# Performance work log

Hardware: AMD Instinct MI355X
Metric: run time of the kernel (lower is better)

The kernel has to match this reference:

```python
import jax, jax.numpy as jnp
import numpy as np

ENT_TOTAL = 1_000_000
REL_TOTAL = 10_000
HIDDEN = 128      # == ent_size == rel_size
REL_TYPE = 1_000
MARGIN = 1.0
BATCH = 8192


def setup_inputs() -> dict:
    key = jax.random.key(0)
    ks = jax.random.split(key, 10)
    return {
        "ent_emb": jax.random.normal(ks[0], (ENT_TOTAL, HIDDEN), jnp.float32) * 0.05,
        "rel_emb": jax.random.normal(ks[1], (REL_TOTAL, HIDDEN), jnp.float32) * 0.05,
        "type_mat": jax.random.normal(ks[2], (REL_TYPE, HIDDEN * HIDDEN), jnp.float32) * 0.05,
        "pos_h": jax.random.randint(ks[3], (BATCH,), 0, ENT_TOTAL, jnp.int64 if jax.config.jax_enable_x64 else jnp.int32),
        "pos_t": jax.random.randint(ks[4], (BATCH,), 0, ENT_TOTAL, jnp.int32),
        "pos_r": jax.random.randint(ks[5], (BATCH,), 0, REL_TOTAL, jnp.int32),
        "pos_type_r": jax.random.randint(ks[6], (BATCH,), 0, REL_TYPE, jnp.int32),
        "neg_h": jax.random.randint(ks[7], (BATCH,), 0, ENT_TOTAL, jnp.int32),
        "neg_t": jax.random.randint(ks[8], (BATCH,), 0, ENT_TOTAL, jnp.int32),
        "neg_r": jax.random.randint(ks[9], (BATCH,), 0, REL_TOTAL, jnp.int32),
    }


def _l2norm(x):
    return x * jax.lax.rsqrt(jnp.sum(x * x, axis=-1, keepdims=True) + 1e-12)


def _calc(h, t, r):
    # l2-normalize each, then |h + r - t|
    return jnp.abs(_l2norm(h) + _l2norm(r) - _l2norm(t))


def reference(ent_emb, rel_emb, type_mat, pos_h, pos_t, pos_r, pos_type_r,
              neg_h, neg_t, neg_r):
    B = pos_h.shape[0]
    D = ent_emb.shape[1]
    # gathers
    p_h = ent_emb[pos_h]                       # [B, D]
    p_t = ent_emb[pos_t]
    p_r = rel_emb[pos_r]
    n_h = ent_emb[neg_h]
    n_t = ent_emb[neg_t]
    n_r = rel_emb[neg_r]
    # per-sample transfer matrix; original code uses pos_type_r for BOTH
    # positive and negative (faithful to source).
    T = type_mat[pos_type_r].reshape(B, D, D)  # [B, ent_size, rel_size]
    # per-sample transfer: [B, D] x [B, D, R] -> [B, R]
    p_h_ = jnp.einsum('bd,bdr->br', p_h, T)
    p_t_ = jnp.einsum('bd,bdr->br', p_t, T)
    n_h_ = jnp.einsum('bd,bdr->br', n_h, T)
    n_t_ = jnp.einsum('bd,bdr->br', n_t, T)
    p_score = jnp.sum(_calc(p_h_, p_t_, p_r), axis=-1, keepdims=True)  # [B,1]
    n_score = jnp.sum(_calc(n_h_, n_t_, n_r), axis=-1, keepdims=True)
    loss = jnp.mean(jnp.maximum(p_score - n_score + MARGIN, 0.0))
    return loss
```

## Files before the change

### kernel.cpp

```cpp
#include <hip/hip_runtime.h>

#define D 128
#define MAX_B 8192
#define MARGIN 1.0f


#define BFLY5(x) { x += __shfl_xor(x, 1); x += __shfl_xor(x, 2); x += __shfl_xor(x, 4); \
                   x += __shfl_xor(x, 8); x += __shfl_xor(x, 16); }

#define FMA4(A, T, S) { (A).x = fmaf((T).x, (S), (A).x); (A).y = fmaf((T).y, (S), (A).y); \
                        (A).z = fmaf((T).z, (S), (A).z); (A).w = fmaf((T).w, (S), (A).w); }

struct SampleRegs {
    float2 e0, e1, e2, e3;
    float4 rp, rn;
};

__device__ __forceinline__ void fetch_sample(
    SampleRegs& S, int o,
    const float* __restrict__ ent, const float* __restrict__ rel,
    const int* __restrict__ pos_h, const int* __restrict__ pos_t,
    const int* __restrict__ pos_r, const int* __restrict__ neg_h,
    const int* __restrict__ neg_t, const int* __restrict__ neg_r,
    int l, int cg)
{
    const size_t b0 = (size_t)pos_h[o] * D;
    const size_t b1 = (size_t)pos_t[o] * D;
    const size_t b2 = (size_t)neg_h[o] * D;
    const size_t b3 = (size_t)neg_t[o] * D;
    const size_t r0 = (size_t)pos_r[o] * D;
    const size_t r1 = (size_t)neg_r[o] * D;
    S.e0 = *(const float2*)&ent[b0 + 2 * l];
    S.e1 = *(const float2*)&ent[b1 + 2 * l];
    S.e2 = *(const float2*)&ent[b2 + 2 * l];
    S.e3 = *(const float2*)&ent[b3 + 2 * l];
    S.rp = *(const float4*)&rel[r0 + 4 * cg];
    S.rn = *(const float4*)&rel[r1 + 4 * cg];
}

__device__ __forceinline__ void commit_sample(float* vbw, const SampleRegs& S, int l) {
    *(float2*)&vbw[0 * D + 2 * l] = S.e0;
    *(float2*)&vbw[1 * D + 2 * l] = S.e1;
    *(float2*)&vbw[2 * D + 2 * l] = S.e2;
    *(float2*)&vbw[3 * D + 2 * l] = S.e3;
}

__device__ __forceinline__ float sample_score(
    const float* __restrict__ T_lds, const float* __restrict__ vbw,
    int h, int cg, float4 rp, float4 rn)
{
    const float4* __restrict__ T4 = (const float4*)T_lds;
    const float4* __restrict__ vv = (const float4*)vbw;
    float4 a0 = make_float4(0.f, 0.f, 0.f, 0.f), a1 = a0, a2 = a0, a3 = a0;
    const int rb  = h * 64;
    const int vb0 = h * 16;
    #pragma unroll 4
    for (int dg = 0; dg < 16; ++dg) {
        const int row = rb + dg * 4;
        const float4 t0 = T4[(row + 0) * 32 + cg];
        const float4 t1 = T4[(row + 1) * 32 + cg];
        const float4 t2 = T4[(row + 2) * 32 + cg];
        const float4 t3 = T4[(row + 3) * 32 + cg];
        const int vi = vb0 + dg;
        const float4 v0 = vv[0 * 32 + vi];
        FMA4(a0, t0, v0.x); FMA4(a0, t1, v0.y); FMA4(a0, t2, v0.z); FMA4(a0, t3, v0.w);
        const float4 v1 = vv[1 * 32 + vi];
        FMA4(a1, t0, v1.x); FMA4(a1, t1, v1.y); FMA4(a1, t2, v1.z); FMA4(a1, t3, v1.w);
        const float4 v2 = vv[2 * 32 + vi];
        FMA4(a2, t0, v2.x); FMA4(a2, t1, v2.y); FMA4(a2, t2, v2.z); FMA4(a2, t3, v2.w);
        const float4 v3 = vv[3 * 32 + vi];
        FMA4(a3, t0, v3.x); FMA4(a3, t1, v3.y); FMA4(a3, t2, v3.z); FMA4(a3, t3, v3.w);
    }
    a0.x += __shfl_xor(a0.x, 32); a0.y += __shfl_xor(a0.y, 32);
    a0.z += __shfl_xor(a0.z, 32); a0.w += __shfl_xor(a0.w, 32);
    a1.x += __shfl_xor(a1.x, 32); a1.y += __shfl_xor(a1.y, 32);
    a1.z += __shfl_xor(a1.z, 32); a1.w += __shfl_xor(a1.w, 32);
    a2.x += __shfl_xor(a2.x, 32); a2.y += __shfl_xor(a2.y, 32);
    a2.z += __shfl_xor(a2.z, 32); a2.w += __shfl_xor(a2.w, 32);
    a3.x += __shfl_xor(a3.x, 32); a3.y += __shfl_xor(a3.y, 32);
    a3.z += __shfl_xor(a3.z, 32); a3.w += __shfl_xor(a3.w, 32);

    float sph = a0.x*a0.x + a0.y*a0.y + a0.z*a0.z + a0.w*a0.w;
    float spt = a1.x*a1.x + a1.y*a1.y + a1.z*a1.z + a1.w*a1.w;
    float snh = a2.x*a2.x + a2.y*a2.y + a2.z*a2.z + a2.w*a2.w;
    float snt = a3.x*a3.x + a3.y*a3.y + a3.z*a3.z + a3.w*a3.w;
    float spr = rp.x*rp.x + rp.y*rp.y + rp.z*rp.z + rp.w*rp.w;
    float snr = rn.x*rn.x + rn.y*rn.y + rn.z*rn.z + rn.w*rn.w;
    BFLY5(sph); BFLY5(spt); BFLY5(snh); BFLY5(snt); BFLY5(spr); BFLY5(snr);
    const float iph = rsqrtf(sph + 1e-12f);
    const float ipt = rsqrtf(spt + 1e-12f);
    const float inh = rsqrtf(snh + 1e-12f);
    const float itn = rsqrtf(snt + 1e-12f);
    const float ipr = rsqrtf(spr + 1e-12f);
    const float inr = rsqrtf(snr + 1e-12f);
    float z = fabsf(a0.x*iph + rp.x*ipr - a1.x*ipt)
            + fabsf(a0.y*iph + rp.y*ipr - a1.y*ipt)
            + fabsf(a0.z*iph + rp.z*ipr - a1.z*ipt)
            + fabsf(a0.w*iph + rp.w*ipr - a1.w*ipt)
            - fabsf(a2.x*inh + rn.x*inr - a3.x*itn)
            - fabsf(a2.y*inh + rn.y*inr - a3.y*itn)
            - fabsf(a2.z*inh + rn.z*inr - a3.z*itn)
            - fabsf(a2.w*inh + rn.w*inr - a3.w*itn);
    BFLY5(z);
    return fmaxf(z + MARGIN, 0.f);
}

__global__ __launch_bounds__(512, 4) void fused_kernel(
    const float* __restrict__ ent,
    const float* __restrict__ rel,
    const float* __restrict__ tmat,
    const int* __restrict__ pos_h,
    const int* __restrict__ pos_t,
    const int* __restrict__ pos_r,
    const int* __restrict__ type_r,
    const int* __restrict__ neg_h,
    const int* __restrict__ neg_t,
    const int* __restrict__ neg_r,
    float* __restrict__ out,
    int B, float inv_B)
{
    const int t   = blockIdx.x;
    const int tid = threadIdx.x;
    const int l   = tid & 63;
    const int w   = tid >> 6;
    const int cg  = l & 31;
    const int h   = l >> 5;

    __shared__ float T_lds[D * D];
    __shared__ float vbuf[8][4][D];
    int* lsc = (int*)&vbuf[0][0][0];

    float4 ts[8];
    {
        const float4* Tg = (const float4*)(tmat + (size_t)t * (D * D));
        #pragma unroll
        for (int k = 0; k < 8; ++k)
            ts[k] = Tg[tid + k * 512];
    }

    const int per = (B + 511) >> 9;
    int vals[16];
    const int base = tid * per;
    int mc = 0;
    if (per == 16 && base + 15 < B) {
        const int4* vp = (const int4*)(type_r + base);
        #pragma unroll
        for (int k = 0; k < 4; ++k) {
            const int4 v = vp[k];
            vals[4*k+0] = v.x; vals[4*k+1] = v.y;
            vals[4*k+2] = v.z; vals[4*k+3] = v.w;
        }
    } else {
        for (int j = 0; j < 16; ++j) {
            const int s = base + j;
            vals[j] = (j < per && s < B) ? type_r[s] : -1;
        }
    }
    #pragma unroll
    for (int j = 0; j < 16; ++j) mc += (vals[j] == t);

    {
        float4* Ts = (float4*)T_lds;
        #pragma unroll
        for (int k = 0; k < 8; ++k)
            Ts[tid + k * 512] = ts[k];
    }

    int inc = mc;
    #pragma unroll
    for (int off = 1; off < 64; off <<= 1) {
        const int tv = __shfl_up(inc, off);
        if (l >= off) inc += tv;
    }
    if (l == 63) lsc[64 + w] = inc;
    __syncthreads();
    int wbase = 0, cnt = 0;
    #pragma unroll
    for (int k = 0; k < 8; ++k) {
        const int s = lsc[64 + k];
        wbase += (k < w) ? s : 0;
        cnt += s;
    }
    const int excl = wbase + inc - mc;
    __syncthreads();

    float wl = 0.f;
    for (int r0 = 0;; r0 += 64) {
        {
            int g = excl;
            #pragma unroll
            for (int j = 0; j < 16; ++j) {
                if (vals[j] == t) {
                    const int wr = g - r0;
                    if (wr >= 0 && wr < 64) lsc[wr] = base + j;
                    ++g;
                }
            }
        }
        __syncthreads();
        const int wcnt = min(cnt - r0, 64);
        int sidx[8];
        int nk = 0;
        #pragma unroll
        for (int k = 0; k < 8; ++k) {
            const int rank = w + 8 * k;
            if (rank < wcnt) sidx[nk++] = lsc[rank];
        }
        __syncthreads();

        if (nk > 0) {
            float* vbw = &vbuf[w][0][0];
            SampleRegs A, Bq;
            fetch_sample(A, sidx[0], ent, rel, pos_h, pos_t, pos_r,
                         neg_h, neg_t, neg_r, l, cg);
            for (int k = 0;; ++k) {
                commit_sample(vbw, A, l);
                const bool more = (k + 1) < nk;
                if (more)
                    fetch_sample(Bq, sidx[k + 1], ent, rel, pos_h, pos_t, pos_r,
                                 neg_h, neg_t, neg_r, l, cg);
                wl += sample_score(T_lds, vbw, h, cg, A.rp, A.rn);
                if (!more) break;
                A = Bq;
            }
        }
        if (r0 + 64 >= cnt) break;
        __syncthreads();
    }

    __syncthreads();
    if (l == 0) ((float*)lsc)[w] = wl;
    __syncthreads();
    if (tid == 0) {
        float s = 0.f;
        #pragma unroll
        for (int k = 0; k < 8; ++k) s += ((float*)lsc)[k];
        if (s != 0.f) atomicAdd(out, s * inv_B);
    }
}


__global__ __launch_bounds__(128) void transr_fallback(
    const float* __restrict__ ent, const float* __restrict__ rel,
    const float* __restrict__ tmat,
    const int* __restrict__ pos_h, const int* __restrict__ pos_t,
    const int* __restrict__ pos_r, const int* __restrict__ pos_type_r,
    const int* __restrict__ neg_h, const int* __restrict__ neg_t,
    const int* __restrict__ neg_r, float* __restrict__ out, int B)
{
    const int b = blockIdx.x;
    const int r = threadIdx.x;
    const int lane = r & 63;
    const int wid = r >> 6;
    __shared__ float4 vcomb[D];
    __shared__ float sred[16];
    vcomb[r] = make_float4(ent[(size_t)pos_h[b]*D + r], ent[(size_t)pos_t[b]*D + r],
                           ent[(size_t)neg_h[b]*D + r], ent[(size_t)neg_t[b]*D + r]);
    const float prr = rel[(size_t)pos_r[b] * D + r];
    const float nrr = rel[(size_t)neg_r[b] * D + r];
    __syncthreads();
    const float* __restrict__ T = tmat + (size_t)pos_type_r[b] * (D * D);
    float aph = 0.f, apt = 0.f, anh = 0.f, ant = 0.f;
    #pragma unroll 8
    for (int d = 0; d < D; ++d) {
        const float t = T[d * D + r];
        const float4 v = vcomb[d];
        aph = fmaf(v.x, t, aph); apt = fmaf(v.y, t, apt);
        anh = fmaf(v.z, t, anh); ant = fmaf(v.w, t, ant);
    }
    float s0 = aph*aph, s1 = apt*apt, s2 = anh*anh, s3 = ant*ant;
    float s4 = prr*prr, s5 = nrr*nrr;
    #pragma unroll
    for (int off = 32; off; off >>= 1) {
        s0 += __shfl_xor(s0, off); s1 += __shfl_xor(s1, off);
        s2 += __shfl_xor(s2, off); s3 += __shfl_xor(s3, off);
        s4 += __shfl_xor(s4, off); s5 += __shfl_xor(s5, off);
    }
    if (lane == 0) {
        sred[wid*8+0]=s0; sred[wid*8+1]=s1; sred[wid*8+2]=s2;
        sred[wid*8+3]=s3; sred[wid*8+4]=s4; sred[wid*8+5]=s5;
    }
    __syncthreads();
    const float iph = rsqrtf(sred[0]+sred[8] +1e-12f);
    const float ipt = rsqrtf(sred[1]+sred[9] +1e-12f);
    const float inh = rsqrtf(sred[2]+sred[10]+1e-12f);
    const float itn = rsqrtf(sred[3]+sred[11]+1e-12f);
    const float ipr = rsqrtf(sred[4]+sred[12]+1e-12f);
    const float inr = rsqrtf(sred[5]+sred[13]+1e-12f);
    float pterm = fabsf(aph*iph + prr*ipr - apt*ipt);
    float nterm = fabsf(anh*inh + nrr*inr - ant*itn);
    #pragma unroll
    for (int off = 32; off; off >>= 1) {
        pterm += __shfl_xor(pterm, off);
        nterm += __shfl_xor(nterm, off);
    }
    __syncthreads();
    if (lane == 0) { sred[wid*2+0] = pterm; sred[wid*2+1] = nterm; }
    __syncthreads();
    if (r == 0)
        atomicAdd(out, fmaxf(sred[0]+sred[2] - sred[1]-sred[3] + MARGIN, 0.f) / (float)B);
}


extern "C" void kernel_launch(void* const* d_in, const int* in_sizes, int n_in,
                              void* d_out, int out_size, void* d_ws, size_t ws_size,
                              hipStream_t stream) {
    const float* ent  = (const float*)d_in[0];
    const float* rel  = (const float*)d_in[1];
    const float* tmat = (const float*)d_in[2];
    const int* pos_h      = (const int*)d_in[3];
    const int* pos_t      = (const int*)d_in[4];
    const int* pos_r      = (const int*)d_in[5];
    const int* pos_type_r = (const int*)d_in[6];
    const int* neg_h      = (const int*)d_in[7];
    const int* neg_t      = (const int*)d_in[8];
    const int* neg_r      = (const int*)d_in[9];
    float* out = (float*)d_out;
    const int B = in_sizes[3];
    const int ntype = in_sizes[2] / (D * D);

    hipMemsetAsync(out, 0, sizeof(float), stream);

    if (B > MAX_B) {
        transr_fallback<<<B, 128, 0, stream>>>(
            ent, rel, tmat, pos_h, pos_t, pos_r, pos_type_r,
            neg_h, neg_t, neg_r, out, B);
        return;
    }

    fused_kernel<<<ntype, 512, 0, stream>>>(
        ent, rel, tmat, pos_h, pos_t, pos_r, pos_type_r,
        neg_h, neg_t, neg_r, out, B, 1.0f / (float)B);
}
```

Baseline: 46.61 us.

## Process two relation types per block to halve grid size

Each block now handles two consecutive relation types. It counts matches for both in a single pass over type_r, packing the two counts into one int so a single prefix scan serves both. The second type's transfer matrix is loaded into LDS after the first type's samples are scored. This halves the repeated per-block scan of the 8192-entry type array and the block launch count. The cost is less parallelism (500 blocks instead of 1000) and serialized matrix loads within each block.

```diff
diff --git a/kernel.cpp b/kernel.cpp
--- a/kernel.cpp
+++ b/kernel.cpp
@@ -117,9 +117,10 @@
     const int* __restrict__ neg_t,
     const int* __restrict__ neg_r,
     float* __restrict__ out,
-    int B, float inv_B)
+    int B, int ntype, float inv_B)
 {
-    const int t   = blockIdx.x;
+    const int t0  = 2 * blockIdx.x;
+    const int t1  = t0 + 1;
     const int tid = threadIdx.x;
     const int l   = tid & 63;
     const int w   = tid >> 6;
@@ -132,7 +133,7 @@
 
     float4 ts[8];
     {
-        const float4* Tg = (const float4*)(tmat + (size_t)t * (D * D));
+        const float4* Tg = (const float4*)(tmat + (size_t)t0 * (D * D));
         #pragma unroll
         for (int k = 0; k < 8; ++k)
             ts[k] = Tg[tid + k * 512];
@@ -141,7 +142,7 @@
     const int per = (B + 511) >> 9;
     int vals[16];
     const int base = tid * per;
-    int mc = 0;
+    int mc0 = 0, mc1 = 0;
     if (per == 16 && base + 15 < B) {
         const int4* vp = (const int4*)(type_r + base);
         #pragma unroll
@@ -157,7 +158,10 @@
         }
     }
     #pragma unroll
-    for (int j = 0; j < 16; ++j) mc += (vals[j] == t);
+    for (int j = 0; j < 16; ++j) {
+        mc0 += (vals[j] == t0);
+        mc1 += (vals[j] == t1);
+    }
 
     {
         float4* Ts = (float4*)T_lds;
@@ -166,7 +170,8 @@
             Ts[tid + k * 512] = ts[k];
     }
 
-    int inc = mc;
+    const int p = mc0 | (mc1 << 16);
+    int inc = p;
     #pragma unroll
     for (int off = 1; off < 64; off <<= 1) {
         const int tv = __shfl_up(inc, off);
@@ -174,58 +179,79 @@
     }
     if (l == 63) lsc[64 + w] = inc;
     __syncthreads();
-    int wbase = 0, cnt = 0;
+    int wbase = 0, tot = 0;
     #pragma unroll
     for (int k = 0; k < 8; ++k) {
         const int s = lsc[64 + k];
         wbase += (k < w) ? s : 0;
-        cnt += s;
-    }
-    const int excl = wbase + inc - mc;
+        tot += s;
+    }
+    const int epk  = wbase + inc - p;
+    const int excl0 = epk & 0xFFFF, excl1 = (int)((unsigned)epk >> 16);
+    const int cnt0  = tot & 0xFFFF, cnt1  = (int)((unsigned)tot >> 16);
     __syncthreads();
 
     float wl = 0.f;
-    for (int r0 = 0;; r0 += 64) {
-        {
-            int g = excl;
+
+    for (int ph = 0; ph < 2; ++ph) {
+        const int t    = ph ? t1 : t0;
+        const int excl = ph ? excl1 : excl0;
+        const int cnt  = ph ? cnt1 : cnt0;
+        if (ph == 1) {
+            if (t >= ntype || cnt == 0) break;
+            const float4* Tg = (const float4*)(tmat + (size_t)t * (D * D));
+            float4 t2[8];
             #pragma unroll
-            for (int j = 0; j < 16; ++j) {
-                if (vals[j] == t) {
-                    const int wr = g - r0;
-                    if (wr >= 0 && wr < 64) lsc[wr] = base + j;
-                    ++g;
+            for (int k = 0; k < 8; ++k) t2[k] = Tg[tid + k * 512];
+            __syncthreads();
+            float4* Ts = (float4*)T_lds;
+            #pragma unroll
+            for (int k = 0; k < 8; ++k) Ts[tid + k * 512] = t2[k];
+        }
+        if (cnt == 0) continue;
+
+        for (int r0 = 0;; r0 += 64) {
+            {
+                int g = excl;
+                #pragma unroll
+                for (int j = 0; j < 16; ++j) {
+                    if (vals[j] == t) {
+                        const int wr = g - r0;
+                        if (wr >= 0 && wr < 64) lsc[wr] = base + j;
+                        ++g;
+                    }
                 }
             }
+            __syncthreads();
+            const int wcnt = min(cnt - r0, 64);
+            int sidx[8];
+            int nk = 0;
+            #pragma unroll
+            for (int k = 0; k < 8; ++k) {
+                const int rank = w + 8 * k;
+                if (rank < wcnt) sidx[nk++] = lsc[rank];
+            }
+            __syncthreads();
+
+            if (nk > 0) {
+                float* vbw = &vbuf[w][0][0];
+                SampleRegs A, Bq;
+                fetch_sample(A, sidx[0], ent, rel, pos_h, pos_t, pos_r,
+                             neg_h, neg_t, neg_r, l, cg);
+                for (int k = 0;; ++k) {
+                    commit_sample(vbw, A, l);
+                    const bool more = (k + 1) < nk;
+                    if (more)
+                        fetch_sample(Bq, sidx[k + 1], ent, rel, pos_h, pos_t,
+                                     pos_r, neg_h, neg_t, neg_r, l, cg);
+                    wl += sample_score(T_lds, vbw, h, cg, A.rp, A.rn);
+                    if (!more) break;
+                    A = Bq;
+                }
+            }
+            if (r0 + 64 >= cnt) break;
+            __syncthreads();
         }
-        __syncthreads();
-        const int wcnt = min(cnt - r0, 64);
-        int sidx[8];
-        int nk = 0;
-        #pragma unroll
-        for (int k = 0; k < 8; ++k) {
-            const int rank = w + 8 * k;
-            if (rank < wcnt) sidx[nk++] = lsc[rank];
-        }
-        __syncthreads();
-
-        if (nk > 0) {
-            float* vbw = &vbuf[w][0][0];
-            SampleRegs A, Bq;
-            fetch_sample(A, sidx[0], ent, rel, pos_h, pos_t, pos_r,
-                         neg_h, neg_t, neg_r, l, cg);
-            for (int k = 0;; ++k) {
-                commit_sample(vbw, A, l);
-                const bool more = (k + 1) < nk;
-                if (more)
-                    fetch_sample(Bq, sidx[k + 1], ent, rel, pos_h, pos_t, pos_r,
-                                 neg_h, neg_t, neg_r, l, cg);
-                wl += sample_score(T_lds, vbw, h, cg, A.rp, A.rn);
-                if (!more) break;
-                A = Bq;
-            }
-        }
-        if (r0 + 64 >= cnt) break;
-        __syncthreads();
     }
 
     __syncthreads();
@@ -263,10 +289,10 @@
     float aph = 0.f, apt = 0.f, anh = 0.f, ant = 0.f;
     #pragma unroll 8
     for (int d = 0; d < D; ++d) {
-        const float t = T[d * D + r];
+        const float tt = T[d * D + r];
         const float4 v = vcomb[d];
-        aph = fmaf(v.x, t, aph); apt = fmaf(v.y, t, apt);
-        anh = fmaf(v.z, t, anh); ant = fmaf(v.w, t, ant);
+        aph = fmaf(v.x, tt, aph); apt = fmaf(v.y, tt, apt);
+        anh = fmaf(v.z, tt, anh); ant = fmaf(v.w, tt, ant);
     }
     float s0 = aph*aph, s1 = apt*apt, s2 = anh*anh, s3 = ant*ant;
     float s4 = prr*prr, s5 = nrr*nrr;
@@ -328,7 +354,7 @@
         return;
     }
 
-    fused_kernel<<<ntype, 512, 0, stream>>>(
+    fused_kernel<<<(ntype + 1) / 2, 512, 0, stream>>>(
         ent, rel, tmat, pos_h, pos_t, pos_r, pos_type_r,
-        neg_h, neg_t, neg_r, out, B, 1.0f / (float)B);
-}
+        neg_h, neg_t, neg_r, out, B, ntype, 1.0f / (float)B);
+}
```

New measurement: 55.22 us. +18.5%, slower.
